# Kernel tuning notes

Hardware: AMD Instinct MI355X
Metric: run time of the kernel (lower is better)

## Reference

```python
import jax, jax.numpy as jnp
import numpy as np

B, S, D, U, L, DEG = 32, 256, 256, 256, 16, 16
N = B * S
E = N * DEG


def _xavier(k, shape, fan_in, fan_out):
    return jax.random.normal(k, shape, jnp.float32) * np.float32(np.sqrt(2.0 / (fan_in + fan_out)))


def setup_inputs() -> dict:
    key = jax.random.key(0)
    ks = jax.random.split(key, 16)
    src = jax.random.normal(ks[0], (S, B, D), jnp.float32)
    V_in = _xavier(ks[1], (L, D, U), D, U)
    b_in = jnp.zeros((L, U), jnp.float32)
    V_in_gate = _xavier(ks[2], (D, 1), D, 1)
    b_in_gate = jnp.ones((L, 1), jnp.float32)
    V_out = _xavier(ks[3], (L, D, U), D, U)
    b_out = jnp.zeros((L, U), jnp.float32)
    V_out_gate = _xavier(ks[4], (D, 1), D, 1)
    b_out_gate = jnp.ones((L, 1), jnp.float32)
    W_self_loop = _xavier(ks[5], (D, U), D, U)
    W_self_loop_gate = _xavier(ks[6], (D, 1), D, 1)
    arc_tensor_in = jnp.stack([jax.random.randint(ks[7], (E,), 0, B),
                               jax.random.randint(ks[8], (E,), 0, S)]).astype(jnp.int64)
    arc_tensor_out = jnp.stack([jax.random.randint(ks[9], (E,), 0, B),
                                jax.random.randint(ks[10], (E,), 0, S)]).astype(jnp.int64)
    label_tensor_in = jax.random.randint(ks[11], (1, E), 0, L).astype(jnp.int64)
    label_tensor_out = jax.random.randint(ks[12], (1, E), 0, L).astype(jnp.int64)
    mask_in = jnp.ones((N, DEG), jnp.float32)
    mask_out = jnp.ones((N, DEG), jnp.float32)
    mask_loop = jnp.ones((N, 1), jnp.float32)
    sent_mask = jnp.ones((S, B), jnp.float32)
    return {"src": src, "V_in": V_in, "b_in": b_in, "V_in_gate": V_in_gate,
            "b_in_gate": b_in_gate, "V_out": V_out, "b_out": b_out,
            "V_out_gate": V_out_gate, "b_out_gate": b_out_gate,
            "W_self_loop": W_self_loop, "W_self_loop_gate": W_self_loop_gate,
            "arc_tensor_in": arc_tensor_in, "arc_tensor_out": arc_tensor_out,
            "label_tensor_in": label_tensor_in, "label_tensor_out": label_tensor_out,
            "mask_in": mask_in, "mask_out": mask_out, "mask_loop": mask_loop,
            "sent_mask": sent_mask}


def _gcn_forward(src, V_in, b_in, V_in_gate, b_in_gate, V_out, b_out, V_out_gate,
                 b_out_gate, W_self_loop, W_self_loop_gate, mask_in, mask_out,
                 mask_loop, sent_mask, arc_tensor_in, arc_tensor_out,
                 label_tensor_in, label_tensor_out):
    S_, B_, D_ = src.shape
    U_ = V_in.shape[-1]
    enc = jnp.transpose(src, (1, 0, 2))            # [B,S,D]
    x = enc.reshape(B_ * S_, D_)                   # [N,D]

    def arc_branch(V, b, Vg, bg, arc, lab):
        # per-label transform of all nodes, as in the original: [L,N,U]
        all_lab = jnp.einsum('nd,ldu->lnu', x, V)
        idx = arc[0] * S_ + arc[1]                 # [E] flat node indices
        l = lab[0]                                  # [E] edge labels
        feats = all_lab[l, idx] + b[l]              # [E,U]
        deg = idx.shape[0] // (B_ * S_)
        feats = feats.reshape(B_, S_, deg, U_)
        g = (x @ Vg)[idx, 0] + bg[l, 0]             # [E]
        gate = g.reshape(B_, S_, deg)
        return feats, gate

    in_, in_gate = arc_branch(V_in, b_in, V_in_gate, b_in_gate, arc_tensor_in, label_tensor_in)
    out_, out_gate = arc_branch(V_out, b_out, V_out_gate, b_out_gate, arc_tensor_out, label_tensor_out)
    same = (x @ W_self_loop).reshape(B_, S_, 1, U_)
    same_gate = (x @ W_self_loop_gate).reshape(B_, S_, 1)

    pot = jnp.concatenate([in_, out_, same], axis=2)            # [B,S,maxdeg,U]
    pot_gate = jnp.concatenate([in_gate, out_gate, same_gate], axis=2)
    mask_soft = jnp.concatenate([mask_in, mask_out, mask_loop], axis=1)  # [N,maxdeg]
    md = pot.shape[2]
    pot = pot.reshape(B_ * S_, md, U_)
    probs = jax.nn.sigmoid(pot_gate.reshape(B_ * S_, md)) * mask_soft
    res = jax.nn.relu(jnp.sum(pot * probs[:, :, None], axis=1)).reshape(B_, S_, U_)
    res = res * sent_mask.T[:, :, None]
    return jnp.transpose(res, (1, 0, 2))            # [S,B,U]


def reference(src, V_in, b_in, V_in_gate, b_in_gate, V_out, b_out, V_out_gate,
              b_out_gate, W_self_loop, W_self_loop_gate, arc_tensor_in,
              arc_tensor_out, label_tensor_in, label_tensor_out, mask_in,
              mask_out, mask_loop, sent_mask):
    return _gcn_forward(src, V_in, b_in, V_in_gate, b_in_gate, V_out, b_out,
                        V_out_gate, b_out_gate, W_self_loop, W_self_loop_gate,
                        mask_in, mask_out, mask_loop, sent_mask,
                        arc_tensor_in, arc_tensor_out, label_tensor_in,
                        label_tensor_out)
```

## Files before the change

### kernel.cpp

```cpp
#include <hip/hip_runtime.h>
#include <hip/hip_bf16.h>

#define BB 32
#define SS 256
#define DD 256
#define UU 256
#define LL 16
#define DEG 16
#define NN (BB * SS)
#define EE (NN * DEG)
#define NSLICE 33

using short8 = __attribute__((ext_vector_type(8))) short;
using f32x4  = __attribute__((ext_vector_type(4))) float;

#define GLDS(g, l)                                                        \
  __builtin_amdgcn_global_load_lds(                                       \
      (const __attribute__((address_space(1))) void*)(g),                 \
      (__attribute__((address_space(3))) void*)(l), 16, 0, 0)

__device__ __forceinline__ float bf2f(unsigned short v) {
  union { unsigned u; float f; } t;
  t.u = ((unsigned)v) << 16;
  return t.f;
}

__global__ __launch_bounds__(256) void k_prep(
    const float* __restrict__ src, const float* __restrict__ gin,
    const float* __restrict__ gout, const float* __restrict__ gloop,
    __hip_bfloat16* __restrict__ x_bf, float* __restrict__ xg_in,
    float* __restrict__ xg_out, float* __restrict__ xg_loop) {
  int n = blockIdx.x;
  int b = n / SS, s = n % SS;
  int d = threadIdx.x;
  float v = src[(size_t)(s * BB + b) * DD + d];
  x_bf[(size_t)n * DD + d] = __float2bfloat16(v);
  float p0 = v * gin[d], p1 = v * gout[d], p2 = v * gloop[d];
#pragma unroll
  for (int o = 32; o > 0; o >>= 1) {
    p0 += __shfl_down(p0, o);
    p1 += __shfl_down(p1, o);
    p2 += __shfl_down(p2, o);
  }
  __shared__ float r0[4], r1[4], r2[4];
  int w = threadIdx.x >> 6, lane = threadIdx.x & 63;
  if (lane == 0) { r0[w] = p0; r1[w] = p1; r2[w] = p2; }
  __syncthreads();
  if (threadIdx.x == 0) {
    xg_in[n]   = r0[0] + r0[1] + r0[2] + r0[3];
    xg_out[n]  = r1[0] + r1[1] + r1[2] + r1[3];
    xg_loop[n] = r2[0] + r2[1] + r2[2] + r2[3];
  }
}

__global__ void k_transpose(const float* __restrict__ Vin,
                            const float* __restrict__ Vout,
                            const float* __restrict__ Wself,
                            __hip_bfloat16* __restrict__ Vt) {
  __shared__ float t[32][33];
  int z = blockIdx.z;
  const float* srcM = (z == 0) ? Wself
                    : (z <= LL ? Vin  + (size_t)(z - 1)      * DD * UU
                               : Vout + (size_t)(z - 1 - LL) * DD * UU);
  __hip_bfloat16* dstM = Vt + (size_t)z * UU * DD;
  int u0 = blockIdx.x * 32, d0 = blockIdx.y * 32;
  int tx = threadIdx.x, ty = threadIdx.y;
#pragma unroll
  for (int i = 0; i < 4; i++) {
    int dr = ty + i * 8;
    t[dr][tx] = srcM[(size_t)(d0 + dr) * UU + u0 + tx];
  }
  __syncthreads();
#pragma unroll
  for (int i = 0; i < 4; i++) {
    int ur = ty + i * 8;
    dstM[(size_t)(u0 + ur) * DD + d0 + tx] = __float2bfloat16(t[tx][ur]);
  }
}

__global__ __launch_bounds__(256) void k_gemm(
    const __hip_bfloat16* __restrict__ A, const __hip_bfloat16* __restrict__ Vt,
    const float* __restrict__ b_in, const float* __restrict__ b_out,
    __hip_bfloat16* __restrict__ buf, int z0) {
  __shared__ __align__(16) __hip_bfloat16 As[128 * 32];
  __shared__ __align__(16) __hip_bfloat16 Bs[128 * 32];
  int slice = z0 + blockIdx.z;
  const __hip_bfloat16* Bt = Vt + (size_t)slice * UU * DD;
  __hip_bfloat16* C = buf + (size_t)blockIdx.z * NN * UU;
  const float* bias = nullptr;
  if (slice >= 1 && slice <= LL) bias = b_in + (size_t)(slice - 1) * UU;
  else if (slice > LL)           bias = b_out + (size_t)(slice - 1 - LL) * UU;

  int row0 = blockIdx.x * 128, col0 = blockIdx.y * 128;
  int tid = threadIdx.x;
  int w = tid >> 6, lane = tid & 63;
  int wr = (w >> 1) * 64, wc = (w & 1) * 64;
  int lrow = lane & 15, quad = lane >> 4;
  int sr = lane >> 2;
  int sc = (lane & 3) * 8;

  f32x4 acc[4][4] = {};
  for (int k0 = 0; k0 < DD; k0 += 32) {
#pragma unroll
    for (int t = 0; t < 2; t++) {
      int rb = (w * 2 + t) * 16;
      GLDS(&A[(size_t)(row0 + rb + sr) * DD + k0 + sc], &As[rb * 32]);
      GLDS(&Bt[(size_t)(col0 + rb + sr) * DD + k0 + sc], &Bs[rb * 32]);
    }
    __syncthreads();
    short8 af[4], bfr[4];
#pragma unroll
    for (int i = 0; i < 4; i++)
      af[i] = *(const short8*)&As[(wr + i * 16 + lrow) * 32 + quad * 8];
#pragma unroll
    for (int j = 0; j < 4; j++)
      bfr[j] = *(const short8*)&Bs[(wc + j * 16 + lrow) * 32 + quad * 8];
#pragma unroll
    for (int i = 0; i < 4; i++)
#pragma unroll
      for (int j = 0; j < 4; j++)
        acc[i][j] = __builtin_amdgcn_mfma_f32_16x16x32_bf16(af[i], bfr[j], acc[i][j], 0, 0, 0);
    __syncthreads();
  }
#pragma unroll
  for (int j = 0; j < 4; j++) {
    int col = col0 + wc + j * 16 + lrow;
    float bv = bias ? bias[col] : 0.f;
#pragma unroll
    for (int i = 0; i < 4; i++) {
      int rowb = row0 + wr + i * 16 + quad * 4;
#pragma unroll
      for (int r = 0; r < 4; r++)
        C[(size_t)(rowb + r) * UU + col] = __float2bfloat16(acc[i][j][r] + bv);
    }
  }
}

__global__ __launch_bounds__(64) void k_fuse(
    const __hip_bfloat16* __restrict__ buf,
    const float* __restrict__ b_ing, const float* __restrict__ b_outg,
    const float* __restrict__ xg_in, const float* __restrict__ xg_out,
    const float* __restrict__ xg_loop,
    const int* __restrict__ arc_in, const int* __restrict__ arc_out,
    const int* __restrict__ lab_in, const int* __restrict__ lab_out,
    const float* __restrict__ mask_in, const float* __restrict__ mask_out,
    const float* __restrict__ mask_loop, const float* __restrict__ sent,
    float* __restrict__ out) {
  __shared__ int s_src[32];
  __shared__ int s_slice[32];
  __shared__ float s_w[32];
  int n = blockIdx.x, tid = threadIdx.x;
  if (tid < 32) {
    int br = tid >> 4, k = tid & 15;
    int e = n * DEG + k;
    const int* a = br ? arc_out : arc_in;
    int l = (br ? lab_out : lab_in)[e];
    int srcn = a[e] * SS + a[EE + e];
    float g = (br ? xg_out : xg_in)[srcn] + (br ? b_outg : b_ing)[l];
    float wv = (1.f / (1.f + __expf(-g))) * (br ? mask_out : mask_in)[e];
    s_src[tid] = srcn;
    s_slice[tid] = 1 + br * LL + l;
    s_w[tid] = wv;
  }
  __syncthreads();
  int u4 = tid * 4;
  float a0, a1, a2, a3;
  {
    float wl = (1.f / (1.f + __expf(-xg_loop[n]))) * mask_loop[n];
    ushort4 v = *(const ushort4*)&buf[(size_t)n * UU + u4];
    a0 = wl * bf2f(v.x); a1 = wl * bf2f(v.y);
    a2 = wl * bf2f(v.z); a3 = wl * bf2f(v.w);
  }
#pragma unroll
  for (int k = 0; k < 32; k++) {
    float wv = s_w[k];
    ushort4 v = *(const ushort4*)&buf[((size_t)s_slice[k] * NN + s_src[k]) * UU + u4];
    a0 += wv * bf2f(v.x); a1 += wv * bf2f(v.y);
    a2 += wv * bf2f(v.z); a3 += wv * bf2f(v.w);
  }
  int s = n % SS, b = n / SS;
  float sm = sent[s * BB + b];
  float4 o;
  o.x = fmaxf(a0, 0.f) * sm; o.y = fmaxf(a1, 0.f) * sm;
  o.z = fmaxf(a2, 0.f) * sm; o.w = fmaxf(a3, 0.f) * sm;
  *(float4*)&out[((size_t)s * BB + b) * UU + u4] = o;
}

__global__ __launch_bounds__(64) void k_resinit(
    const __hip_bfloat16* __restrict__ bufS, const float* __restrict__ xg_loop,
    const float* __restrict__ mask_loop, float* __restrict__ res) {
  int n = blockIdx.x, u4 = threadIdx.x * 4;
  float wl = (1.f / (1.f + __expf(-xg_loop[n]))) * mask_loop[n];
  ushort4 v = *(const ushort4*)&bufS[(size_t)n * UU + u4];
  float4 r;
  r.x = wl * bf2f(v.x); r.y = wl * bf2f(v.y);
  r.z = wl * bf2f(v.z); r.w = wl * bf2f(v.w);
  *(float4*)&res[(size_t)n * UU + u4] = r;
}

__global__ __launch_bounds__(64) void k_scatter_acc(
    const __hip_bfloat16* __restrict__ buf,
    const float* __restrict__ b_ing, const float* __restrict__ b_outg,
    const float* __restrict__ xg_in, const float* __restrict__ xg_out,
    const int* __restrict__ arc_in, const int* __restrict__ arc_out,
    const int* __restrict__ lab_in, const int* __restrict__ lab_out,
    const float* __restrict__ mask_in, const float* __restrict__ mask_out,
    float* __restrict__ res, int c0, int c1) {
  __shared__ int s_src[32];
  __shared__ int s_slice[32];
  __shared__ float s_w[32];
  int n = blockIdx.x, tid = threadIdx.x;
  if (tid < 32) {
    int br = tid >> 4, k = tid & 15;
    int e = n * DEG + k;
    const int* a = br ? arc_out : arc_in;
    int l = (br ? lab_out : lab_in)[e];
    int srcn = a[e] * SS + a[EE + e];
    float g = (br ? xg_out : xg_in)[srcn] + (br ? b_outg : b_ing)[l];
    float wv = (1.f / (1.f + __expf(-g))) * (br ? mask_out : mask_in)[e];
    int sl = 1 + br * LL + l;
    s_src[tid] = srcn;
    s_slice[tid] = sl;
    s_w[tid] = (sl >= c0 && sl < c1) ? wv : 0.f;
  }
  __syncthreads();
  int u4 = tid * 4;
  float a0 = 0, a1 = 0, a2 = 0, a3 = 0;
  for (int k = 0; k < 32; k++) {
    float wv = s_w[k];
    if (wv != 0.f) {
      ushort4 v = *(const ushort4*)&buf[((size_t)(s_slice[k] - c0) * NN + s_src[k]) * UU + u4];
      a0 += wv * bf2f(v.x); a1 += wv * bf2f(v.y);
      a2 += wv * bf2f(v.z); a3 += wv * bf2f(v.w);
    }
  }
  float4* rp = (float4*)&res[(size_t)n * UU + u4];
  float4 r = *rp;
  r.x += a0; r.y += a1; r.z += a2; r.w += a3;
  *rp = r;
}

__global__ __launch_bounds__(64) void k_finish(const float* __restrict__ res,
                                               const float* __restrict__ sent,
                                               float* __restrict__ out) {
  int n = blockIdx.x, u4 = threadIdx.x * 4;
  int s = n % SS, b = n / SS;
  float sm = sent[s * BB + b];
  float4 v = *(const float4*)&res[(size_t)n * UU + u4];
  float4 o;
  o.x = fmaxf(v.x, 0.f) * sm; o.y = fmaxf(v.y, 0.f) * sm;
  o.z = fmaxf(v.z, 0.f) * sm; o.w = fmaxf(v.w, 0.f) * sm;
  *(float4*)&out[((size_t)s * BB + b) * UU + u4] = o;
}

extern "C" void kernel_launch(void* const* d_in, const int* in_sizes, int n_in,
                              void* d_out, int out_size, void* d_ws, size_t ws_size,
                              hipStream_t stream) {
  const float* src      = (const float*)d_in[0];
  const float* V_in     = (const float*)d_in[1];
  const float* b_in     = (const float*)d_in[2];
  const float* V_ing    = (const float*)d_in[3];
  const float* b_ing    = (const float*)d_in[4];
  const float* V_out    = (const float*)d_in[5];
  const float* b_out    = (const float*)d_in[6];
  const float* V_outg   = (const float*)d_in[7];
  const float* b_outg   = (const float*)d_in[8];
  const float* W_self   = (const float*)d_in[9];
  const float* W_selfg  = (const float*)d_in[10];
  const int* arc_in     = (const int*)d_in[11];
  const int* arc_out    = (const int*)d_in[12];
  const int* lab_in     = (const int*)d_in[13];
  const int* lab_out    = (const int*)d_in[14];
  const float* mask_in  = (const float*)d_in[15];
  const float* mask_out = (const float*)d_in[16];
  const float* mask_loop= (const float*)d_in[17];
  const float* sent     = (const float*)d_in[18];
  float* out = (float*)d_out;

  char* ws = (char*)d_ws;
  size_t off = 0;
  auto alloc = [&](size_t bytes) -> void* {
    void* p = ws + off;
    off += (bytes + 255) & ~(size_t)255;
    return p;
  };
  __hip_bfloat16* x_bf = (__hip_bfloat16*)alloc((size_t)NN * DD * 2);
  __hip_bfloat16* Vt   = (__hip_bfloat16*)alloc((size_t)NSLICE * UU * DD * 2);
  float* xg_in   = (float*)alloc(NN * 4);
  float* xg_out  = (float*)alloc(NN * 4);
  float* xg_loop = (float*)alloc(NN * 4);

  const size_t slice_b = (size_t)NN * UU * 2;
  size_t remain = ws_size > off ? ws_size - off : 0;

  k_prep<<<NN, 256, 0, stream>>>(src, V_ing, V_outg, W_selfg, x_bf, xg_in, xg_out, xg_loop);
  k_transpose<<<dim3(UU / 32, DD / 32, NSLICE), dim3(32, 8), 0, stream>>>(
      V_in, V_out, W_self, Vt);

  if (remain >= NSLICE * slice_b) {
    __hip_bfloat16* buf = (__hip_bfloat16*)alloc(NSLICE * slice_b);
    k_gemm<<<dim3(NN / 128, UU / 128, NSLICE), 256, 0, stream>>>(
        x_bf, Vt, b_in, b_out, buf, 0);
    k_fuse<<<NN, 64, 0, stream>>>(buf, b_ing, b_outg, xg_in, xg_out, xg_loop,
                                  arc_in, arc_out, lab_in, lab_out,
                                  mask_in, mask_out, mask_loop, sent, out);
  } else {
    float* res = (float*)alloc((size_t)NN * UU * 4);
    __hip_bfloat16* bufS = (__hip_bfloat16*)alloc(slice_b);
    size_t rem2 = ws_size > off ? ws_size - off : 0;
    int C = (int)(rem2 / slice_b);
    if (C > 32) C = 32;
    if (C < 1) C = 1;
    __hip_bfloat16* bufC = (__hip_bfloat16*)alloc((size_t)C * slice_b);

    k_gemm<<<dim3(NN / 128, UU / 128, 1), 256, 0, stream>>>(
        x_bf, Vt, b_in, b_out, bufS, 0);
    k_resinit<<<NN, 64, 0, stream>>>(bufS, xg_loop, mask_loop, res);
    for (int c0 = 1; c0 < NSLICE; c0 += C) {
      int lc = NSLICE - c0 < C ? NSLICE - c0 : C;
      k_gemm<<<dim3(NN / 128, UU / 128, lc), 256, 0, stream>>>(
          x_bf, Vt, b_in, b_out, bufC, c0);
      k_scatter_acc<<<NN, 64, 0, stream>>>(bufC, b_ing, b_outg, xg_in, xg_out,
                                           arc_in, arc_out, lab_in, lab_out,
                                           mask_in, mask_out, res, c0, c0 + lc);
    }
    k_finish<<<NN, 64, 0, stream>>>(res, sent, out);
  }
}
```

Baseline: 196.3 us.

## Aggregate inputs per label before GEMM, fold biases into one wide K-split GEMM

Reorders the computation so neighbour features are gathered and summed per edge-label slice first (k_agg builds a [N, 33*256+128] bf16 matrix, with per-slice gate-weight sums standing in for the bias terms). A single GEMM against concatenated transposed weights, with the biases appended as extra K rows, then produces the result, split over K into 4 fp32 partials that k_finish reduces with relu and the sentence mask. This drops the 33 full per-slice projection outputs and the later random gathers over them, in exchange for a much larger K dimension, a large Y intermediate, and a partial-sum buffer. The aggregation is rounded to bf16 before the matmul, which changes numerics.

```diff
diff --git a/kernel.cpp b/kernel.cpp
--- a/kernel.cpp
+++ b/kernel.cpp
@@ -10,6 +10,10 @@
 #define NN (BB * SS)
 #define EE (NN * DEG)
 #define NSLICE 33
+#define KMAIN (NSLICE * DD)
+#define KTOT  (KMAIN + 128)
+#define KSPLIT 4
+#define KS (KTOT / KSPLIT)
 
 using short8 = __attribute__((ext_vector_type(8))) short;
 using f32x4  = __attribute__((ext_vector_type(4))) float;
@@ -23,6 +27,9 @@
   union { unsigned u; float f; } t;
   t.u = ((unsigned)v) << 16;
   return t.f;
+}
+__device__ __forceinline__ float sigm(float x) {
+  return 1.f / (1.f + __expf(-x));
 }
 
 __global__ __launch_bounds__(256) void k_prep(
@@ -62,7 +69,6 @@
   const float* srcM = (z == 0) ? Wself
                     : (z <= LL ? Vin  + (size_t)(z - 1)      * DD * UU
                                : Vout + (size_t)(z - 1 - LL) * DD * UU);
-  __hip_bfloat16* dstM = Vt + (size_t)z * UU * DD;
   int u0 = blockIdx.x * 32, d0 = blockIdx.y * 32;
   int tx = threadIdx.x, ty = threadIdx.y;
 #pragma unroll
@@ -74,81 +80,35 @@
 #pragma unroll
   for (int i = 0; i < 4; i++) {
     int ur = ty + i * 8;
-    dstM[(size_t)(u0 + ur) * DD + d0 + tx] = __float2bfloat16(t[tx][ur]);
-  }
-}
-
-__global__ __launch_bounds__(256) void k_gemm(
-    const __hip_bfloat16* __restrict__ A, const __hip_bfloat16* __restrict__ Vt,
+    Vt[(size_t)(u0 + ur) * KTOT + z * DD + d0 + tx] = __float2bfloat16(t[tx][ur]);
+  }
+}
+
+__global__ __launch_bounds__(128) void k_biasfill(
     const float* __restrict__ b_in, const float* __restrict__ b_out,
-    __hip_bfloat16* __restrict__ buf, int z0) {
-  __shared__ __align__(16) __hip_bfloat16 As[128 * 32];
-  __shared__ __align__(16) __hip_bfloat16 Bs[128 * 32];
-  int slice = z0 + blockIdx.z;
-  const __hip_bfloat16* Bt = Vt + (size_t)slice * UU * DD;
-  __hip_bfloat16* C = buf + (size_t)blockIdx.z * NN * UU;
-  const float* bias = nullptr;
-  if (slice >= 1 && slice <= LL) bias = b_in + (size_t)(slice - 1) * UU;
-  else if (slice > LL)           bias = b_out + (size_t)(slice - 1 - LL) * UU;
-
-  int row0 = blockIdx.x * 128, col0 = blockIdx.y * 128;
-  int tid = threadIdx.x;
-  int w = tid >> 6, lane = tid & 63;
-  int wr = (w >> 1) * 64, wc = (w & 1) * 64;
-  int lrow = lane & 15, quad = lane >> 4;
-  int sr = lane >> 2;
-  int sc = (lane & 3) * 8;
-
-  f32x4 acc[4][4] = {};
-  for (int k0 = 0; k0 < DD; k0 += 32) {
-#pragma unroll
-    for (int t = 0; t < 2; t++) {
-      int rb = (w * 2 + t) * 16;
-      GLDS(&A[(size_t)(row0 + rb + sr) * DD + k0 + sc], &As[rb * 32]);
-      GLDS(&Bt[(size_t)(col0 + rb + sr) * DD + k0 + sc], &Bs[rb * 32]);
-    }
-    __syncthreads();
-    short8 af[4], bfr[4];
-#pragma unroll
-    for (int i = 0; i < 4; i++)
-      af[i] = *(const short8*)&As[(wr + i * 16 + lrow) * 32 + quad * 8];
-#pragma unroll
-    for (int j = 0; j < 4; j++)
-      bfr[j] = *(const short8*)&Bs[(wc + j * 16 + lrow) * 32 + quad * 8];
-#pragma unroll
-    for (int i = 0; i < 4; i++)
-#pragma unroll
-      for (int j = 0; j < 4; j++)
-        acc[i][j] = __builtin_amdgcn_mfma_f32_16x16x32_bf16(af[i], bfr[j], acc[i][j], 0, 0, 0);
-    __syncthreads();
-  }
-#pragma unroll
-  for (int j = 0; j < 4; j++) {
-    int col = col0 + wc + j * 16 + lrow;
-    float bv = bias ? bias[col] : 0.f;
-#pragma unroll
-    for (int i = 0; i < 4; i++) {
-      int rowb = row0 + wr + i * 16 + quad * 4;
-#pragma unroll
-      for (int r = 0; r < 4; r++)
-        C[(size_t)(rowb + r) * UU + col] = __float2bfloat16(acc[i][j][r] + bv);
-    }
-  }
-}
-
-__global__ __launch_bounds__(64) void k_fuse(
-    const __hip_bfloat16* __restrict__ buf,
-    const float* __restrict__ b_ing, const float* __restrict__ b_outg,
+    __hip_bfloat16* __restrict__ Vt) {
+  int u = blockIdx.x, j = threadIdx.x;
+  float v = 0.f;
+  if (j >= 1 && j <= LL)       v = b_in[(j - 1) * UU + u];
+  else if (j > LL && j < NSLICE) v = b_out[(j - 1 - LL) * UU + u];
+  Vt[(size_t)u * KTOT + KMAIN + j] = __float2bfloat16(v);
+}
+
+__global__ __launch_bounds__(256) void k_agg(
+    const __hip_bfloat16* __restrict__ x,
     const float* __restrict__ xg_in, const float* __restrict__ xg_out,
     const float* __restrict__ xg_loop,
+    const float* __restrict__ b_ing, const float* __restrict__ b_outg,
     const int* __restrict__ arc_in, const int* __restrict__ arc_out,
     const int* __restrict__ lab_in, const int* __restrict__ lab_out,
     const float* __restrict__ mask_in, const float* __restrict__ mask_out,
-    const float* __restrict__ mask_loop, const float* __restrict__ sent,
-    float* __restrict__ out) {
+    const float* __restrict__ mask_loop,
+    __hip_bfloat16* __restrict__ Y) {
+  __shared__ float Ya[NSLICE][DD];
   __shared__ int s_src[32];
-  __shared__ int s_slice[32];
+  __shared__ int s_sl[32];
   __shared__ float s_w[32];
+  __shared__ float s_wsum[NSLICE];
   int n = blockIdx.x, tid = threadIdx.x;
   if (tid < 32) {
     int br = tid >> 4, k = tid & 15;
@@ -157,99 +117,103 @@
     int l = (br ? lab_out : lab_in)[e];
     int srcn = a[e] * SS + a[EE + e];
     float g = (br ? xg_out : xg_in)[srcn] + (br ? b_outg : b_ing)[l];
-    float wv = (1.f / (1.f + __expf(-g))) * (br ? mask_out : mask_in)[e];
     s_src[tid] = srcn;
-    s_slice[tid] = 1 + br * LL + l;
-    s_w[tid] = wv;
-  }
-  __syncthreads();
-  int u4 = tid * 4;
-  float a0, a1, a2, a3;
-  {
-    float wl = (1.f / (1.f + __expf(-xg_loop[n]))) * mask_loop[n];
-    ushort4 v = *(const ushort4*)&buf[(size_t)n * UU + u4];
-    a0 = wl * bf2f(v.x); a1 = wl * bf2f(v.y);
-    a2 = wl * bf2f(v.z); a3 = wl * bf2f(v.w);
-  }
-#pragma unroll
+    s_sl[tid] = 1 + br * LL + l;
+    s_w[tid] = sigm(g) * (br ? mask_out : mask_in)[e];
+  }
+  __syncthreads();
+  float wl = sigm(xg_loop[n]) * mask_loop[n];
+  Ya[0][tid] = wl * bf2f(((const unsigned short*)x)[(size_t)n * DD + tid]);
+#pragma unroll
+  for (int i = 1; i < NSLICE; i++) Ya[i][tid] = 0.f;
+#pragma unroll 4
   for (int k = 0; k < 32; k++) {
     float wv = s_w[k];
-    ushort4 v = *(const ushort4*)&buf[((size_t)s_slice[k] * NN + s_src[k]) * UU + u4];
-    a0 += wv * bf2f(v.x); a1 += wv * bf2f(v.y);
-    a2 += wv * bf2f(v.z); a3 += wv * bf2f(v.w);
+    float xv = bf2f(((const unsigned short*)x)[(size_t)s_src[k] * DD + tid]);
+    Ya[s_sl[k]][tid] += wv * xv;
+  }
+  if (tid < NSLICE) {
+    float ws = 0.f;
+#pragma unroll
+    for (int k = 0; k < 32; k++) ws += (s_sl[k] == tid) ? s_w[k] : 0.f;
+    s_wsum[tid] = ws;
+  }
+  __syncthreads();
+  size_t base = (size_t)n * KTOT;
+#pragma unroll
+  for (int i = 0; i < NSLICE; i++)
+    Y[base + i * DD + tid] = __float2bfloat16(Ya[i][tid]);
+  if (tid < 128)
+    Y[base + KMAIN + tid] = __float2bfloat16(tid < NSLICE ? s_wsum[tid] : 0.f);
+}
+
+__global__ __launch_bounds__(256) void k_gemm(
+    const __hip_bfloat16* __restrict__ A, const __hip_bfloat16* __restrict__ Bt,
+    float* __restrict__ partial) {
+  __shared__ __align__(16) __hip_bfloat16 As[128 * 32];
+  __shared__ __align__(16) __hip_bfloat16 Bs[128 * 32];
+  float* P = partial + (size_t)blockIdx.z * NN * UU;
+  int kbeg = blockIdx.z * KS;
+
+  int row0 = blockIdx.x * 128, col0 = blockIdx.y * 128;
+  int tid = threadIdx.x;
+  int w = tid >> 6, lane = tid & 63;
+  int wr = (w >> 1) * 64, wc = (w & 1) * 64;
+  int lrow = lane & 15, quad = lane >> 4;
+  int sr = lane >> 2;
+  int sc = (lane & 3) * 8;
+
+  f32x4 acc[4][4] = {};
+  for (int k0 = kbeg; k0 < kbeg + KS; k0 += 32) {
+#pragma unroll
+    for (int t = 0; t < 2; t++) {
+      int rb = (w * 2 + t) * 16;
+      GLDS(&A[(size_t)(row0 + rb + sr) * KTOT + k0 + sc], &As[rb * 32]);
+      GLDS(&Bt[(size_t)(col0 + rb + sr) * KTOT + k0 + sc], &Bs[rb * 32]);
+    }
+    __syncthreads();
+    short8 af[4], bfr[4];
+#pragma unroll
+    for (int i = 0; i < 4; i++)
+      af[i] = *(const short8*)&As[(wr + i * 16 + lrow) * 32 + quad * 8];
+#pragma unroll
+    for (int j = 0; j < 4; j++)
+      bfr[j] = *(const short8*)&Bs[(wc + j * 16 + lrow) * 32 + quad * 8];
+#pragma unroll
+    for (int i = 0; i < 4; i++)
+#pragma unroll
+      for (int j = 0; j < 4; j++)
+        acc[i][j] = __builtin_amdgcn_mfma_f32_16x16x32_bf16(af[i], bfr[j], acc[i][j], 0, 0, 0);
+    __syncthreads();
+  }
+#pragma unroll
+  for (int i = 0; i < 4; i++)
+#pragma unroll
+    for (int j = 0; j < 4; j++) {
+      int col = col0 + wc + j * 16 + lrow;
+      int rowb = row0 + wr + i * 16 + quad * 4;
+#pragma unroll
+      for (int r = 0; r < 4; r++)
+        P[(size_t)(rowb + r) * UU + col] = acc[i][j][r];
+    }
+}
+
+__global__ __launch_bounds__(64) void k_finish(const float* __restrict__ partial,
+                                               const float* __restrict__ sent,
+                                               float* __restrict__ out) {
+  int n = blockIdx.x, u4 = threadIdx.x * 4;
+  size_t idx = (size_t)n * UU + u4;
+  float4 a = *(const float4*)&partial[idx];
+#pragma unroll
+  for (int z = 1; z < KSPLIT; z++) {
+    float4 b = *(const float4*)&partial[(size_t)z * NN * UU + idx];
+    a.x += b.x; a.y += b.y; a.z += b.z; a.w += b.w;
   }
   int s = n % SS, b = n / SS;
   float sm = sent[s * BB + b];
   float4 o;
-  o.x = fmaxf(a0, 0.f) * sm; o.y = fmaxf(a1, 0.f) * sm;
-  o.z = fmaxf(a2, 0.f) * sm; o.w = fmaxf(a3, 0.f) * sm;
-  *(float4*)&out[((size_t)s * BB + b) * UU + u4] = o;
-}
-
-__global__ __launch_bounds__(64) void k_resinit(
-    const __hip_bfloat16* __restrict__ bufS, const float* __restrict__ xg_loop,
-    const float* __restrict__ mask_loop, float* __restrict__ res) {
-  int n = blockIdx.x, u4 = threadIdx.x * 4;
-  float wl = (1.f / (1.f + __expf(-xg_loop[n]))) * mask_loop[n];
-  ushort4 v = *(const ushort4*)&bufS[(size_t)n * UU + u4];
-  float4 r;
-  r.x = wl * bf2f(v.x); r.y = wl * bf2f(v.y);
-  r.z = wl * bf2f(v.z); r.w = wl * bf2f(v.w);
-  *(float4*)&res[(size_t)n * UU + u4] = r;
-}
-
-__global__ __launch_bounds__(64) void k_scatter_acc(
-    const __hip_bfloat16* __restrict__ buf,
-    const float* __restrict__ b_ing, const float* __restrict__ b_outg,
-    const float* __restrict__ xg_in, const float* __restrict__ xg_out,
-    const int* __restrict__ arc_in, const int* __restrict__ arc_out,
-    const int* __restrict__ lab_in, const int* __restrict__ lab_out,
-    const float* __restrict__ mask_in, const float* __restrict__ mask_out,
-    float* __restrict__ res, int c0, int c1) {
-  __shared__ int s_src[32];
-  __shared__ int s_slice[32];
-  __shared__ float s_w[32];
-  int n = blockIdx.x, tid = threadIdx.x;
-  if (tid < 32) {
-    int br = tid >> 4, k = tid & 15;
-    int e = n * DEG + k;
-    const int* a = br ? arc_out : arc_in;
-    int l = (br ? lab_out : lab_in)[e];
-    int srcn = a[e] * SS + a[EE + e];
-    float g = (br ? xg_out : xg_in)[srcn] + (br ? b_outg : b_ing)[l];
-    float wv = (1.f / (1.f + __expf(-g))) * (br ? mask_out : mask_in)[e];
-    int sl = 1 + br * LL + l;
-    s_src[tid] = srcn;
-    s_slice[tid] = sl;
-    s_w[tid] = (sl >= c0 && sl < c1) ? wv : 0.f;
-  }
-  __syncthreads();
-  int u4 = tid * 4;
-  float a0 = 0, a1 = 0, a2 = 0, a3 = 0;
-  for (int k = 0; k < 32; k++) {
-    float wv = s_w[k];
-    if (wv != 0.f) {
-      ushort4 v = *(const ushort4*)&buf[((size_t)(s_slice[k] - c0) * NN + s_src[k]) * UU + u4];
-      a0 += wv * bf2f(v.x); a1 += wv * bf2f(v.y);
-      a2 += wv * bf2f(v.z); a3 += wv * bf2f(v.w);
-    }
-  }
-  float4* rp = (float4*)&res[(size_t)n * UU + u4];
-  float4 r = *rp;
-  r.x += a0; r.y += a1; r.z += a2; r.w += a3;
-  *rp = r;
-}
-
-__global__ __launch_bounds__(64) void k_finish(const float* __restrict__ res,
-                                               const float* __restrict__ sent,
-                                               float* __restrict__ out) {
-  int n = blockIdx.x, u4 = threadIdx.x * 4;
-  int s = n % SS, b = n / SS;
-  float sm = sent[s * BB + b];
-  float4 v = *(const float4*)&res[(size_t)n * UU + u4];
-  float4 o;
-  o.x = fmaxf(v.x, 0.f) * sm; o.y = fmaxf(v.y, 0.f) * sm;
-  o.z = fmaxf(v.z, 0.f) * sm; o.w = fmaxf(v.w, 0.f) * sm;
+  o.x = fmaxf(a.x, 0.f) * sm; o.y = fmaxf(a.y, 0.f) * sm;
+  o.z = fmaxf(a.z, 0.f) * sm; o.w = fmaxf(a.w, 0.f) * sm;
   *(float4*)&out[((size_t)s * BB + b) * UU + u4] = o;
 }
 
@@ -285,45 +249,20 @@
     return p;
   };
   __hip_bfloat16* x_bf = (__hip_bfloat16*)alloc((size_t)NN * DD * 2);
-  __hip_bfloat16* Vt   = (__hip_bfloat16*)alloc((size_t)NSLICE * UU * DD * 2);
+  __hip_bfloat16* Vt   = (__hip_bfloat16*)alloc((size_t)UU * KTOT * 2);
   float* xg_in   = (float*)alloc(NN * 4);
   float* xg_out  = (float*)alloc(NN * 4);
   float* xg_loop = (float*)alloc(NN * 4);
-
-  const size_t slice_b = (size_t)NN * UU * 2;
-  size_t remain = ws_size > off ? ws_size - off : 0;
+  __hip_bfloat16* Y = (__hip_bfloat16*)alloc((size_t)NN * KTOT * 2);
+  float* partial = (float*)alloc((size_t)KSPLIT * NN * UU * 4);
 
   k_prep<<<NN, 256, 0, stream>>>(src, V_ing, V_outg, W_selfg, x_bf, xg_in, xg_out, xg_loop);
   k_transpose<<<dim3(UU / 32, DD / 32, NSLICE), dim3(32, 8), 0, stream>>>(
       V_in, V_out, W_self, Vt);
-
-  if (remain >= NSLICE * slice_b) {
-    __hip_bfloat16* buf = (__hip_bfloat16*)alloc(NSLICE * slice_b);
-    k_gemm<<<dim3(NN / 128, UU / 128, NSLICE), 256, 0, stream>>>(
-        x_bf, Vt, b_in, b_out, buf, 0);
-    k_fuse<<<NN, 64, 0, stream>>>(buf, b_ing, b_outg, xg_in, xg_out, xg_loop,
-                                  arc_in, arc_out, lab_in, lab_out,
-                                  mask_in, mask_out, mask_loop, sent, out);
-  } else {
-    float* res = (float*)alloc((size_t)NN * UU * 4);
-    __hip_bfloat16* bufS = (__hip_bfloat16*)alloc(slice_b);
-    size_t rem2 = ws_size > off ? ws_size - off : 0;
-    int C = (int)(rem2 / slice_b);
-    if (C > 32) C = 32;
-    if (C < 1) C = 1;
-    __hip_bfloat16* bufC = (__hip_bfloat16*)alloc((size_t)C * slice_b);
-
-    k_gemm<<<dim3(NN / 128, UU / 128, 1), 256, 0, stream>>>(
-        x_bf, Vt, b_in, b_out, bufS, 0);
-    k_resinit<<<NN, 64, 0, stream>>>(bufS, xg_loop, mask_loop, res);
-    for (int c0 = 1; c0 < NSLICE; c0 += C) {
-      int lc = NSLICE - c0 < C ? NSLICE - c0 : C;
-      k_gemm<<<dim3(NN / 128, UU / 128, lc), 256, 0, stream>>>(
-          x_bf, Vt, b_in, b_out, bufC, c0);
-      k_scatter_acc<<<NN, 64, 0, stream>>>(bufC, b_ing, b_outg, xg_in, xg_out,
-                                           arc_in, arc_out, lab_in, lab_out,
-                                           mask_in, mask_out, res, c0, c0 + lc);
-    }
-    k_finish<<<NN, 64, 0, stream>>>(res, sent, out);
-  }
-}
+  k_biasfill<<<UU, 128, 0, stream>>>(b_in, b_out, Vt);
+  k_agg<<<NN, 256, 0, stream>>>(x_bf, xg_in, xg_out, xg_loop, b_ing, b_outg,
+                                arc_in, arc_out, lab_in, lab_out,
+                                mask_in, mask_out, mask_loop, Y);
+  k_gemm<<<dim3(NN / 128, UU / 128, KSPLIT), 256, 0, stream>>>(Y, Vt, partial);
+  k_finish<<<NN, 64, 0, stream>>>(partial, sent, out);
+}
```

Result: slower. 228.1 us (+16.2%).
